# Kernel optimization log

Hardware: AMD Instinct MI355X
Metric: run time of the kernel (lower is better)

The kernel has to match this reference:

```python
import jax, jax.numpy as jnp
import numpy as np

B, N, D, H, F = 16, 512, 768, 8, 96  # D == H*F, dims preserved across layers
NEG_INF = -1e20


def setup_inputs() -> dict:
    key = jax.random.key(0)
    ks = jax.random.split(key, 16)
    embeddings = jax.random.normal(ks[0], (B, N, D), dtype=jnp.float32)
    # 0/1 float adjacency with self-loops so no row is fully masked
    adj = (jax.random.uniform(ks[1], (B, N, N)) < 0.3).astype(jnp.float32)
    adj = jnp.maximum(adj, jnp.eye(N, dtype=jnp.float32)[None])
    convo_len = jnp.full((B,), N, dtype=jnp.int32)

    def layer_params(k0, k1, k2, k3, k4, in_dim, out_dim):
        sW = (2.0 / (in_dim + out_dim)) ** 0.5  # ~xavier
        sa = (2.0 / (out_dim + 1)) ** 0.5
        sH = (2.0 / (in_dim + in_dim)) ** 0.5
        return dict(
            W=jax.random.normal(k0, (H, in_dim, out_dim)) * sW,
            b=jnp.zeros((out_dim,), jnp.float32),
            a_src=jax.random.normal(k1, (H, out_dim, 1)) * sa,
            a_dst=jax.random.normal(k2, (H, out_dim, 1)) * sa,
            Hw=jax.random.normal(k3, (in_dim, in_dim)) * sH,
            Hb=jnp.zeros((in_dim,), jnp.float32),
        )

    p0 = layer_params(ks[2], ks[3], ks[4], ks[5], ks[6], D, F)
    p1 = layer_params(ks[7], ks[8], ks[9], ks[10], ks[11], D, F)
    return {
        "embeddings": embeddings, "adj": adj, "convo_len": convo_len,
        "W0": p0["W"], "b0": p0["b"], "a_src0": p0["a_src"], "a_dst0": p0["a_dst"], "Hw0": p0["Hw"], "Hb0": p0["Hb"],
        "W1": p1["W"], "b1": p1["b"], "a_src1": p1["a_src"], "a_dst1": p1["a_dst"], "Hw1": p1["Hw"], "Hb1": p1["Hb"],
    }


def gat_layer(x, adj, W, b, a_src, a_dst, Hw, Hb):
    b_, n_, _ = x.shape
    h_, _, f_ = W.shape
    h = jnp.einsum('bni,hio->bhno', x, W)            # [B,H,N,F]
    t = jnp.tanh(h)
    s = jnp.einsum('bhno,ho->bhn', t, a_src[..., 0])  # attn_src
    d = jnp.einsum('bhno,ho->bhn', t, a_dst[..., 0])  # attn_dst
    attn = jax.nn.leaky_relu(s[:, :, :, None] + d[:, :, None, :], 0.2)  # [B,H,N,N]
    attn = jnp.where(adj[:, None, :, :] > 0, attn, NEG_INF)
    attn = jax.nn.softmax(attn, axis=-1)
    out = jnp.einsum('bhij,bhjo->bhio', attn, h) + b  # [B,H,N,F]
    # faithful to torch: transpose(0,1).contiguous().view(batch, N, -1)
    out = jnp.transpose(out, (1, 0, 2, 3)).reshape(b_, n_, h_ * f_)
    out = jax.nn.elu(out)
    gate = jax.nn.sigmoid(x @ Hw.T + Hb)
    return gate * out + (1.0 - gate) * x


def reference(embeddings, adj, convo_len,
              W0, b0, a_src0, a_dst0, Hw0, Hb0,
              W1, b1, a_src1, a_dst1, Hw1, Hb1):
    x = gat_layer(embeddings, adj, W0, b0, a_src0, a_dst0, Hw0, Hb0)
    x = gat_layer(x, adj, W1, b1, a_src1, a_dst1, Hw1, Hb1)
    return x
```

## Files before the change

kernel.cpp:

```cpp
#include <hip/hip_runtime.h>
#include <cstdint>
#include <cstddef>

typedef __attribute__((ext_vector_type(4))) float f32x4;
typedef __attribute__((ext_vector_type(8))) __bf16 bf16x8;
typedef __attribute__((ext_vector_type(8))) unsigned short u16x8;
typedef __attribute__((ext_vector_type(4))) unsigned short u16x4;

__device__ __forceinline__ unsigned short f2bf(float f){
  unsigned int u = __float_as_uint(f);
  u += 0x7fffu + ((u >> 16) & 1u);
  return (unsigned short)(u >> 16);
}
__device__ __forceinline__ float bf2f(unsigned short u){
  return __uint_as_float(((unsigned int)u) << 16);
}
__device__ __forceinline__ float fast_tanh(float x){
  const float e = __expf(2.f * x);
  return 1.f - 2.f / (e + 1.f);
}

__device__ __forceinline__ void gload_lds16(const void* g, void* l){
  __builtin_amdgcn_global_load_lds((const __attribute__((address_space(1))) void*)g,
                                   (__attribute__((address_space(3))) void*)l, 16, 0, 0);
}

__device__ __forceinline__ f32x4 mfma16(bf16x8 a, bf16x8 b, f32x4 c){
  return __builtin_amdgcn_mfma_f32_16x16x32_bf16(a, b, c, 0, 0, 0);
}

__global__ __launch_bounds__(256) void prep_kernel(const float* __restrict__ in,
                                                   unsigned short* __restrict__ out,
                                                   const float* __restrict__ adj,
                                                   unsigned int* __restrict__ mask){
  const int bid = blockIdx.x;
  if (bid < 6144){
    int i = bid * 256 + threadIdx.x;
    f32x4 v = ((const f32x4*)in)[i];
    union { unsigned short u[4]; unsigned long long ll; } o;
    #pragma unroll
    for (int e = 0; e < 4; ++e) o.u[e] = f2bf(v[e]);
    ((unsigned long long*)out)[i] = o.ll;
  } else {
    int idx = (bid - 6144) * 256 + threadIdx.x;
    const float* a = adj + (size_t)idx * 32;
    unsigned int m = 0;
    #pragma unroll
    for (int e = 0; e < 8; ++e){
      f32x4 v = *(const f32x4*)(a + e * 4);
      m |= (v[0] > 0.f ? 1u : 0u) << (e * 4);
      m |= (v[1] > 0.f ? 1u : 0u) << (e * 4 + 1);
      m |= (v[2] > 0.f ? 1u : 0u) << (e * 4 + 2);
      m |= (v[3] > 0.f ? 1u : 0u) << (e * 4 + 3);
    }
    mask[idx] = m;
  }
}

__global__ __launch_bounds__(192) void buildBt_kernel(const float* __restrict__ W0,
                                                      const float* __restrict__ Hw0,
                                                      unsigned short* __restrict__ Bt0,
                                                      const float* __restrict__ W1,
                                                      const float* __restrict__ Hw1,
                                                      unsigned short* __restrict__ Bt1){
  const int bid = blockIdx.x;
  const int layer = bid >= 1536;
  const int n = layer ? bid - 1536 : bid;
  const float* W  = layer ? W1  : W0;
  const float* Hw = layer ? Hw1 : Hw0;
  unsigned short* Bt = layer ? Bt1 : Bt0;
  int k4 = threadIdx.x;
  float v[4];
  if (n < 768){
    int head = n / 96, f = n % 96;
    const float* base = W + (size_t)head * 768 * 96 + f;
    #pragma unroll
    for (int e = 0; e < 4; ++e) v[e] = base[(size_t)(k4 * 4 + e) * 96];
  } else {
    f32x4 t = *(const f32x4*)(Hw + (size_t)(n - 768) * 768 + k4 * 4);
    #pragma unroll
    for (int e = 0; e < 4; ++e) v[e] = t[e];
  }
  union { unsigned short u[4]; unsigned long long ll; } o;
  #pragma unroll
  for (int e = 0; e < 4; ++e) o.u[e] = f2bf(v[e]);
  ((unsigned long long*)(Bt + (size_t)n * 768))[k4] = o.ll;
}

__global__ __launch_bounds__(256, 3)
void gemm_kernel(const unsigned short* __restrict__ A,
                 const unsigned short* __restrict__ Bt,
                 const float* __restrict__ Hb,
                 unsigned short* __restrict__ hb,
                 unsigned short* __restrict__ hT,
                 unsigned short* __restrict__ glogit){
  __shared__ __align__(16) char lds[49152];
  const int tid  = threadIdx.x;
  const int wid  = tid >> 6;
  const int lane = tid & 63;
  const int orig = blockIdx.x;
  const int wgid = (orig & 7) * 192 + (orig >> 3);
  const int mtile = wgid / 24, ntile = wgid % 24;
  const int m0 = mtile * 128, n0 = ntile * 64;
  const int wm = (wid >> 1) * 64, wn = (wid & 1) * 32;
  const int g = lane >> 4, r16 = lane & 15;

  auto stage = [&](int kt, char* base){
    #pragma unroll
    for (int c = 0; c < 4; ++c){
      const int ch = c * 256 + tid;
      const int row = ch >> 3, sp = ch & 7;
      const int cj = sp ^ (row & 7);
      gload_lds16(A + (size_t)(m0 + row) * 768 + kt * 64 + cj * 8, base + ch * 16);
    }
    #pragma unroll
    for (int c = 0; c < 2; ++c){
      const int ch = c * 256 + tid;
      const int row = ch >> 3, sp = ch & 7;
      const int cj = sp ^ (row & 7);
      gload_lds16(Bt + (size_t)(n0 + row) * 768 + kt * 64 + cj * 8, base + 16384 + ch * 16);
    }
  };

  f32x4 acc[4][2];
  #pragma unroll
  for (int i = 0; i < 4; ++i)
    #pragma unroll
    for (int j = 0; j < 2; ++j) acc[i][j] = (f32x4){0.f, 0.f, 0.f, 0.f};

  stage(0, lds);
  __syncthreads();

  for (int kt = 0; kt < 12; ++kt){
    const int cur = kt & 1;
    if (kt < 11) stage(kt + 1, lds + (cur ^ 1) * 24576);
    const char* base = lds + cur * 24576;
    bf16x8 af[4][2], bfr[2][2];
    #pragma unroll
    for (int t = 0; t < 4; ++t){
      const int rowA = wm + t * 16 + r16;
      #pragma unroll
      for (int kk = 0; kk < 2; ++kk){
        const int ckk = (kk << 2) | g;
        af[t][kk] = *(const bf16x8*)(base + rowA * 128 + ((ckk ^ (rowA & 7)) << 4));
      }
    }
    #pragma unroll
    for (int nt = 0; nt < 2; ++nt){
      const int rowB = wn + nt * 16 + r16;
      #pragma unroll
      for (int kk = 0; kk < 2; ++kk){
        const int ckk = (kk << 2) | g;
        bfr[nt][kk] = *(const bf16x8*)(base + 16384 + rowB * 128 + ((ckk ^ (rowB & 7)) << 4));
      }
    }
    #pragma unroll
    for (int mt = 0; mt < 4; ++mt)
      #pragma unroll
      for (int nt = 0; nt < 2; ++nt){
        acc[mt][nt] = mfma16(af[mt][0], bfr[nt][0], acc[mt][nt]);
        acc[mt][nt] = mfma16(af[mt][1], bfr[nt][1], acc[mt][nt]);
      }
    __syncthreads();
  }

  if (n0 < 768){
    #pragma unroll
    for (int mt = 0; mt < 4; ++mt){
      #pragma unroll
      for (int nt = 0; nt < 2; ++nt){
        const int n = n0 + wn + nt * 16 + r16;
        const int head = n / 96, f = n % 96;
        #pragma unroll
        for (int r = 0; r < 4; ++r){
          const int m = m0 + wm + mt * 16 + g * 4 + r;
          const unsigned short v = f2bf(acc[mt][nt][r]);
          hb[(size_t)m * 768 + n] = v;
          const int b = m >> 9, node = m & 511;
          hT[(((size_t)(b * 8 + head)) * 96 + f) * 512 + node] = v;
        }
      }
    }
  } else {
    #pragma unroll
    for (int mt = 0; mt < 4; ++mt){
      #pragma unroll
      for (int nt = 0; nt < 2; ++nt){
        const int n = n0 + wn + nt * 16 + r16;
        const float hbv = Hb[n - 768];
        #pragma unroll
        for (int r = 0; r < 4; ++r){
          const int m = m0 + wm + mt * 16 + g * 4 + r;
          glogit[(size_t)m * 768 + (n - 768)] = f2bf(acc[mt][nt][r] + hbv);
        }
      }
    }
  }
}

__global__ __launch_bounds__(256)
void sd_kernel(const unsigned short* __restrict__ h, const float* __restrict__ asrc,
               const float* __restrict__ adst, float* __restrict__ s, float* __restrict__ d){
  const int idx  = blockIdx.x * 4 + (threadIdx.x >> 6);
  const int lane = threadIdx.x & 63;
  const int m = idx >> 3, head = idx & 7;
  const unsigned short* hr = h + (size_t)m * 768 + head * 96;
  const float* as_ = asrc + head * 96;
  const float* ad_ = adst + head * 96;
  float t1 = fast_tanh(bf2f(hr[lane]));
  float ss = t1 * as_[lane];
  float dd = t1 * ad_[lane];
  if (lane < 32){
    float t2 = fast_tanh(bf2f(hr[64 + lane]));
    ss += t2 * as_[64 + lane];
    dd += t2 * ad_[64 + lane];
  }
  #pragma unroll
  for (int o = 32; o > 0; o >>= 1){ ss += __shfl_xor(ss, o); dd += __shfl_xor(dd, o); }
  if (lane == 0){
    const int b = m >> 9, node = m & 511;
    const int o = ((b * 8 + head) << 9) + node;
    s[o] = ss; d[o] = dd;
  }
}

__global__ __launch_bounds__(256)
void attn_kernel(const float* __restrict__ s, const float* __restrict__ d,
                 const unsigned int* __restrict__ mask,
                 const unsigned short* __restrict__ hT,
                 const float* __restrict__ bias,
                 const unsigned short* __restrict__ glogit,
                 const float* __restrict__ xin,
                 float* __restrict__ outf,
                 unsigned short* __restrict__ outb,
                 int write_b){
  const int idx = blockIdx.x;
  const int bh = idx & 127, ib = idx >> 7;
  const int b  = bh >> 3;
  const int tid = threadIdx.x, wid = tid >> 6, lane = tid & 63;
  const int g = lane >> 4, r16 = lane & 15;
  const int rowbase = ib * 64 + wid * 16;

  __shared__ float d_lds[512];
  __shared__ float bias_lds[96];
  __shared__ __align__(16) char vbuf[2][12288];
  float* att_s = (float*)vbuf;

  const float* dv = d + bh * 512;
  if (tid < 128) ((f32x4*)d_lds)[tid] = ((const f32x4*)dv)[tid];
  if (tid >= 128 && tid < 152) ((f32x4*)bias_lds)[tid - 128] = ((const f32x4*)bias)[tid - 128];

  const unsigned short* hTb = hT + (size_t)bh * 96 * 512;

  auto stage = [&](int p, int bufi){
    #pragma unroll
    for (int ss2 = 0; ss2 < 3; ++ss2){
      const int ch = ss2 * 256 + tid;
      const int row = ch >> 3, slotpos = ch & 7;
      const int cj = slotpos ^ (row & 7);
      gload_lds16(hTb + (size_t)row * 512 + p * 64 + cj * 8, vbuf[bufi] + ch * 16);
    }
  };

  const int i_mine = rowbase + r16;
  const float s_i = s[bh * 512 + i_mine];

  unsigned int mw[16];
  {
    const uint4* mrow = (const uint4*)(mask + ((size_t)b * 512 + i_mine) * 16);
    uint4 a0 = mrow[0], a1 = mrow[1], a2 = mrow[2], a3 = mrow[3];
    mw[0]=a0.x; mw[1]=a0.y; mw[2]=a0.z; mw[3]=a0.w;
    mw[4]=a1.x; mw[5]=a1.y; mw[6]=a1.z; mw[7]=a1.w;
    mw[8]=a2.x; mw[9]=a2.y; mw[10]=a2.z; mw[11]=a2.w;
    mw[12]=a3.x; mw[13]=a3.y; mw[14]=a3.z; mw[15]=a3.w;
  }

  stage(0, 0);
  __syncthreads();

  float Mx = d_lds[lane];
  #pragma unroll
  for (int t = 1; t < 8; ++t) Mx = fmaxf(Mx, d_lds[t * 64 + lane]);
  #pragma unroll
  for (int o = 32; o > 0; o >>= 1) Mx = fmaxf(Mx, __shfl_xor(Mx, o));
  const float scm = s_i + Mx;
  const float m_i = fmaxf(scm, 0.2f * scm);

  f32x4 acc2[6];
  #pragma unroll
  for (int ft = 0; ft < 6; ++ft) acc2[ft] = (f32x4){0.f, 0.f, 0.f, 0.f};
  float L = 0.f;

  for (int p = 0; p < 8; ++p){
    if (p < 7) stage(p + 1, (p + 1) & 1);
    const char* vb = vbuf[p & 1];
    #pragma unroll
    for (int half = 0; half < 2; ++half){
      const int jt = p * 2 + half;
      const unsigned int w = mw[jt];
      const int j8 = jt * 32 + g * 8;
      f32x4 dA = *(const f32x4*)(d_lds + j8);
      f32x4 dB = *(const f32x4*)(d_lds + j8 + 4);
      u16x8 pa;
      #pragma unroll
      for (int e = 0; e < 4; ++e){
        float sc = s_i + dA[e]; sc = fmaxf(sc, 0.2f * sc);
        float p1 = ((w >> (g * 8 + e)) & 1u) ? __expf(sc - m_i) : 0.f;
        L += p1; pa[e] = f2bf(p1);
        float sc2 = s_i + dB[e]; sc2 = fmaxf(sc2, 0.2f * sc2);
        float p2 = ((w >> (g * 8 + 4 + e)) & 1u) ? __expf(sc2 - m_i) : 0.f;
        L += p2; pa[4 + e] = f2bf(p2);
      }
      const bf16x8 af = __builtin_bit_cast(bf16x8, pa);
      const int slot = ((half * 4 + g) ^ (r16 & 7)) * 16;
      #pragma unroll
      for (int ft = 0; ft < 6; ++ft){
        bf16x8 vf = *(const bf16x8*)(vb + (ft * 16 + r16) * 128 + slot);
        acc2[ft] = mfma16(af, vf, acc2[ft]);
      }
    }
    __syncthreads();
  }

  L += __shfl_xor(L, 16);
  L += __shfl_xor(L, 32);
  const float linv = 1.f / L;
  float lr[4];
  #pragma unroll
  for (int r = 0; r < 4; ++r) lr[r] = __shfl(linv, g * 4 + r);

  #pragma unroll
  for (int ft = 0; ft < 6; ++ft){
    const int f = ft * 16 + r16;
    const float bv = bias_lds[f];
    #pragma unroll
    for (int r = 0; r < 4; ++r){
      const int node = rowbase + g * 4 + r;
      att_s[((node >> 3) & 7) * 768 + (node & 7) * 96 + f] = acc2[ft][r] * lr[r] + bv;
    }
  }
  __syncthreads();

  const int hh = bh & 7;
  const int bb2 = (hh << 1) | (b >> 3);
  const int mbase = bb2 * 512 + ((b & 7) << 6) + ib * 8;
  const size_t gb4 = (size_t)mbase * 192;
  #pragma unroll
  for (int sgi = 0; sgi < 6; ++sgi){
    const int ei = sgi * 256 + tid;
    f32x4 a4 = ((const f32x4*)att_s)[ei];
    u16x4 gl = ((const u16x4*)glogit)[gb4 + ei];
    f32x4 xv = ((const f32x4*)xin)[gb4 + ei];
    f32x4 o;
    #pragma unroll
    for (int e = 0; e < 4; ++e){
      const float gate = 1.f / (1.f + __expf(-bf2f(gl[e])));
      const float a = a4[e];
      const float eluv = a > 0.f ? a : (__expf(a) - 1.f);
      o[e] = gate * eluv + (1.f - gate) * xv[e];
    }
    ((f32x4*)outf)[gb4 + ei] = o;
    if (write_b){
      union { unsigned short u[4]; unsigned long long ll; } ob;
      #pragma unroll
      for (int e = 0; e < 4; ++e) ob.u[e] = f2bf(o[e]);
      ((unsigned long long*)outb)[gb4 + ei] = ob.ll;
    }
  }
}

extern "C" void kernel_launch(void* const* d_in, const int* in_sizes, int n_in,
                              void* d_out, int out_size, void* d_ws, size_t ws_size,
                              hipStream_t stream){
  const float* emb   = (const float*)d_in[0];
  const float* adj   = (const float*)d_in[1];
  const float* W0    = (const float*)d_in[3];
  const float* b0    = (const float*)d_in[4];
  const float* asrc0 = (const float*)d_in[5];
  const float* adst0 = (const float*)d_in[6];
  const float* Hw0   = (const float*)d_in[7];
  const float* Hb0   = (const float*)d_in[8];
  const float* W1    = (const float*)d_in[9];
  const float* b1    = (const float*)d_in[10];
  const float* asrc1 = (const float*)d_in[11];
  const float* adst1 = (const float*)d_in[12];
  const float* Hw1   = (const float*)d_in[13];
  const float* Hb1   = (const float*)d_in[14];

  char* ws = (char*)d_ws;
  size_t off = 0;
  auto alloc = [&](size_t bytes){ void* p = ws + off; off += (bytes + 255) & ~(size_t)255; return p; };
  unsigned short* x0b  = (unsigned short*)alloc(8192ull * 768 * 2);
  unsigned short* Bt0  = (unsigned short*)alloc(1536ull * 768 * 2);
  unsigned short* Bt1  = (unsigned short*)alloc(1536ull * 768 * 2);
  unsigned short* hb   = (unsigned short*)alloc(8192ull * 768 * 2);
  unsigned short* hT   = (unsigned short*)alloc(8192ull * 768 * 2);
  unsigned short* glogit = (unsigned short*)alloc(8192ull * 768 * 2);
  float* sbuf          = (float*)alloc(65536ull * 4);
  float* dbuf          = (float*)alloc(65536ull * 4);
  float* x1            = (float*)alloc(8192ull * 768 * 4);
  unsigned int* mask   = (unsigned int*)alloc(16ull * 512 * 16 * 4);
  (void)ws_size; (void)in_sizes; (void)n_in; (void)out_size;

  prep_kernel<<<6656, 256, 0, stream>>>(emb, x0b, adj, mask);
  buildBt_kernel<<<3072, 192, 0, stream>>>(W0, Hw0, Bt0, W1, Hw1, Bt1);

  gemm_kernel<<<1536, 256, 0, stream>>>(x0b, Bt0, Hb0, hb, hT, glogit);
  sd_kernel<<<16384, 256, 0, stream>>>(hb, asrc0, adst0, sbuf, dbuf);
  attn_kernel<<<1024, 256, 0, stream>>>(sbuf, dbuf, mask, hT, b0, glogit, emb, x1, x0b, 1);

  gemm_kernel<<<1536, 256, 0, stream>>>(x0b, Bt1, Hb1, hb, hT, glogit);
  sd_kernel<<<16384, 256, 0, stream>>>(hb, asrc1, adst1, sbuf, dbuf);
  attn_kernel<<<1024, 256, 0, stream>>>(sbuf, dbuf, mask, hT, b1, glogit, x1, (float*)d_out, x0b, 0);
}
```

Baseline: 288.4 us.

## Stage GEMM epilogue through LDS, drop hb buffer, rework sd kernel, merge prep

The GEMM epilogue now writes its tile into swizzled LDS and then issues 16-byte coalesced stores for both hT and glogit, replacing scattered 2-byte stores. The row-major hb copy is removed, and sd_kernel reads the transposed hT directly, with one block per (batch, head) and its attention vectors held in LDS. buildBt is merged into prep_kernel to save a launch, and s_setprio is raised around the MFMA loop in attention. The risks are extra LDS traffic and barriers in the epilogue, and that sd now runs only 128 blocks, which may underfill the GPU.

```diff
diff --git a/kernel.cpp b/kernel.cpp
--- a/kernel.cpp
+++ b/kernel.cpp
@@ -32,7 +32,13 @@
 __global__ __launch_bounds__(256) void prep_kernel(const float* __restrict__ in,
                                                    unsigned short* __restrict__ out,
                                                    const float* __restrict__ adj,
-                                                   unsigned int* __restrict__ mask){
+                                                   unsigned int* __restrict__ mask,
+                                                   const float* __restrict__ W0,
+                                                   const float* __restrict__ Hw0,
+                                                   unsigned short* __restrict__ Bt0,
+                                                   const float* __restrict__ W1,
+                                                   const float* __restrict__ Hw1,
+                                                   unsigned short* __restrict__ Bt1){
   const int bid = blockIdx.x;
   if (bid < 6144){
     int i = bid * 256 + threadIdx.x;
@@ -41,7 +47,7 @@
     #pragma unroll
     for (int e = 0; e < 4; ++e) o.u[e] = f2bf(v[e]);
     ((unsigned long long*)out)[i] = o.ll;
-  } else {
+  } else if (bid < 6656){
     int idx = (bid - 6144) * 256 + threadIdx.x;
     const float* a = adj + (size_t)idx * 32;
     unsigned int m = 0;
@@ -54,44 +60,38 @@
       m |= (v[3] > 0.f ? 1u : 0u) << (e * 4 + 3);
     }
     mask[idx] = m;
-  }
-}
-
-__global__ __launch_bounds__(192) void buildBt_kernel(const float* __restrict__ W0,
-                                                      const float* __restrict__ Hw0,
-                                                      unsigned short* __restrict__ Bt0,
-                                                      const float* __restrict__ W1,
-                                                      const float* __restrict__ Hw1,
-                                                      unsigned short* __restrict__ Bt1){
-  const int bid = blockIdx.x;
-  const int layer = bid >= 1536;
-  const int n = layer ? bid - 1536 : bid;
-  const float* W  = layer ? W1  : W0;
-  const float* Hw = layer ? Hw1 : Hw0;
-  unsigned short* Bt = layer ? Bt1 : Bt0;
-  int k4 = threadIdx.x;
-  float v[4];
-  if (n < 768){
-    int head = n / 96, f = n % 96;
-    const float* base = W + (size_t)head * 768 * 96 + f;
-    #pragma unroll
-    for (int e = 0; e < 4; ++e) v[e] = base[(size_t)(k4 * 4 + e) * 96];
   } else {
-    f32x4 t = *(const f32x4*)(Hw + (size_t)(n - 768) * 768 + k4 * 4);
-    #pragma unroll
-    for (int e = 0; e < 4; ++e) v[e] = t[e];
-  }
-  union { unsigned short u[4]; unsigned long long ll; } o;
-  #pragma unroll
-  for (int e = 0; e < 4; ++e) o.u[e] = f2bf(v[e]);
-  ((unsigned long long*)(Bt + (size_t)n * 768))[k4] = o.ll;
+    const int rel = bid - 6656;
+    const int layer = rel >= 1536;
+    const int n = layer ? rel - 1536 : rel;
+    const float* W  = layer ? W1  : W0;
+    const float* Hw = layer ? Hw1 : Hw0;
+    unsigned short* Bt = layer ? Bt1 : Bt0;
+    const int k4 = threadIdx.x;
+    if (k4 < 192){
+      float v[4];
+      if (n < 768){
+        int head = n / 96, f = n % 96;
+        const float* base = W + (size_t)head * 768 * 96 + f;
+        #pragma unroll
+        for (int e = 0; e < 4; ++e) v[e] = base[(size_t)(k4 * 4 + e) * 96];
+      } else {
+        f32x4 t = *(const f32x4*)(Hw + (size_t)(n - 768) * 768 + k4 * 4);
+        #pragma unroll
+        for (int e = 0; e < 4; ++e) v[e] = t[e];
+      }
+      union { unsigned short u[4]; unsigned long long ll; } o;
+      #pragma unroll
+      for (int e = 0; e < 4; ++e) o.u[e] = f2bf(v[e]);
+      ((unsigned long long*)(Bt + (size_t)n * 768))[k4] = o.ll;
+    }
+  }
 }
 
 __global__ __launch_bounds__(256, 3)
 void gemm_kernel(const unsigned short* __restrict__ A,
                  const unsigned short* __restrict__ Bt,
                  const float* __restrict__ Hb,
-                 unsigned short* __restrict__ hb,
                  unsigned short* __restrict__ hT,
                  unsigned short* __restrict__ glogit){
   __shared__ __align__(16) char lds[49152];
@@ -169,59 +169,82 @@
     for (int mt = 0; mt < 4; ++mt){
       #pragma unroll
       for (int nt = 0; nt < 2; ++nt){
-        const int n = n0 + wn + nt * 16 + r16;
-        const int head = n / 96, f = n % 96;
+        const int n_local = wn + nt * 16 + r16;
+        const int m_base  = wm + mt * 16 + g * 4;
+        union { unsigned short u[4]; unsigned long long ll; } pk;
+        #pragma unroll
+        for (int r = 0; r < 4; ++r) pk.u[r] = f2bf(acc[mt][nt][r]);
+        const int byte = m_base * 2;
+        const int chunk = byte >> 4, o = byte & 15;
+        const int pbyte = n_local * 256 + ((chunk ^ (n_local & 15)) << 4) + o;
+        *(unsigned long long*)(lds + pbyte) = pk.ll;
+      }
+    }
+    __syncthreads();
+    const int b_ = m0 >> 9, nodebase = m0 & 511;
+    #pragma unroll
+    for (int it = 0; it < 4; ++it){
+      const int ci = it * 256 + tid;
+      const int row = ci >> 4, l = ci & 15;
+      const int pbyte = row * 256 + (((l ^ (row & 15))) << 4);
+      f32x4 v = *(const f32x4*)(lds + pbyte);
+      const int n = n0 + row, head = n / 96, f = n % 96;
+      *(f32x4*)(hT + (((size_t)(b_ * 8 + head)) * 96 + f) * 512 + nodebase + l * 8) = v;
+    }
+  } else {
+    #pragma unroll
+    for (int mt = 0; mt < 4; ++mt){
+      #pragma unroll
+      for (int nt = 0; nt < 2; ++nt){
+        const int n_local = wn + nt * 16 + r16;
+        const float hbv = Hb[n0 - 768 + n_local];
+        const int c = n_local >> 3;
         #pragma unroll
         for (int r = 0; r < 4; ++r){
-          const int m = m0 + wm + mt * 16 + g * 4 + r;
-          const unsigned short v = f2bf(acc[mt][nt][r]);
-          hb[(size_t)m * 768 + n] = v;
-          const int b = m >> 9, node = m & 511;
-          hT[(((size_t)(b * 8 + head)) * 96 + f) * 512 + node] = v;
+          const int m_local = wm + mt * 16 + g * 4 + r;
+          const int pbyte = m_local * 128 + ((c ^ (m_local & 7)) << 4) + (n_local & 7) * 2;
+          *(unsigned short*)(lds + pbyte) = f2bf(acc[mt][nt][r] + hbv);
         }
       }
     }
-  } else {
-    #pragma unroll
-    for (int mt = 0; mt < 4; ++mt){
-      #pragma unroll
-      for (int nt = 0; nt < 2; ++nt){
-        const int n = n0 + wn + nt * 16 + r16;
-        const float hbv = Hb[n - 768];
-        #pragma unroll
-        for (int r = 0; r < 4; ++r){
-          const int m = m0 + wm + mt * 16 + g * 4 + r;
-          glogit[(size_t)m * 768 + (n - 768)] = f2bf(acc[mt][nt][r] + hbv);
-        }
-      }
+    __syncthreads();
+    const int colbase = n0 - 768;
+    #pragma unroll
+    for (int it = 0; it < 4; ++it){
+      const int ci = it * 256 + tid;
+      const int row = ci >> 3, l = ci & 7;
+      const int pbyte = row * 128 + ((l ^ (row & 7)) << 4);
+      f32x4 v = *(const f32x4*)(lds + pbyte);
+      *(f32x4*)(glogit + (size_t)(m0 + row) * 768 + colbase + l * 8) = v;
     }
   }
 }
 
 __global__ __launch_bounds__(256)
-void sd_kernel(const unsigned short* __restrict__ h, const float* __restrict__ asrc,
+void sd_kernel(const unsigned short* __restrict__ hT, const float* __restrict__ asrc,
                const float* __restrict__ adst, float* __restrict__ s, float* __restrict__ d){
-  const int idx  = blockIdx.x * 4 + (threadIdx.x >> 6);
-  const int lane = threadIdx.x & 63;
-  const int m = idx >> 3, head = idx & 7;
-  const unsigned short* hr = h + (size_t)m * 768 + head * 96;
-  const float* as_ = asrc + head * 96;
-  const float* ad_ = adst + head * 96;
-  float t1 = fast_tanh(bf2f(hr[lane]));
-  float ss = t1 * as_[lane];
-  float dd = t1 * ad_[lane];
-  if (lane < 32){
-    float t2 = fast_tanh(bf2f(hr[64 + lane]));
-    ss += t2 * as_[64 + lane];
-    dd += t2 * ad_[64 + lane];
-  }
-  #pragma unroll
-  for (int o = 32; o > 0; o >>= 1){ ss += __shfl_xor(ss, o); dd += __shfl_xor(dd, o); }
-  if (lane == 0){
-    const int b = m >> 9, node = m & 511;
-    const int o = ((b * 8 + head) << 9) + node;
-    s[o] = ss; d[o] = dd;
-  }
+  const int bh = blockIdx.x;
+  const int tid = threadIdx.x;
+  const int head = bh & 7;
+  __shared__ float as_lds[96], ad_lds[96];
+  if (tid < 96) as_lds[tid] = asrc[head * 96 + tid];
+  else if (tid >= 128 && tid < 224) ad_lds[tid - 128] = adst[head * 96 + tid - 128];
+  __syncthreads();
+
+  const unsigned short* hTb = hT + (size_t)bh * 96 * 512 + tid * 2;
+  float s0 = 0.f, s1 = 0.f, d0 = 0.f, d1 = 0.f;
+  #pragma unroll 8
+  for (int f = 0; f < 96; ++f){
+    const unsigned int u = *(const unsigned int*)(hTb + (size_t)f * 512);
+    const float t0 = fast_tanh(bf2f((unsigned short)(u & 0xffffu)));
+    const float t1 = fast_tanh(bf2f((unsigned short)(u >> 16)));
+    const float a = as_lds[f], dd = ad_lds[f];
+    s0 += t0 * a;  s1 += t1 * a;
+    d0 += t0 * dd; d1 += t1 * dd;
+  }
+  const int o = (bh << 9) + tid * 2;
+  *(float2*)(s + o) = make_float2(s0, s1);
+  *(float2*)(d + o) = make_float2(d0, d1);
 }
 
 __global__ __launch_bounds__(256)
@@ -313,11 +336,13 @@
       }
       const bf16x8 af = __builtin_bit_cast(bf16x8, pa);
       const int slot = ((half * 4 + g) ^ (r16 & 7)) * 16;
+      __builtin_amdgcn_s_setprio(1);
       #pragma unroll
       for (int ft = 0; ft < 6; ++ft){
         bf16x8 vf = *(const bf16x8*)(vb + (ft * 16 + r16) * 128 + slot);
         acc2[ft] = mfma16(af, vf, acc2[ft]);
       }
+      __builtin_amdgcn_s_setprio(0);
     }
     __syncthreads();
   }
@@ -393,7 +418,6 @@
   unsigned short* x0b  = (unsigned short*)alloc(8192ull * 768 * 2);
   unsigned short* Bt0  = (unsigned short*)alloc(1536ull * 768 * 2);
   unsigned short* Bt1  = (unsigned short*)alloc(1536ull * 768 * 2);
-  unsigned short* hb   = (unsigned short*)alloc(8192ull * 768 * 2);
   unsigned short* hT   = (unsigned short*)alloc(8192ull * 768 * 2);
   unsigned short* glogit = (unsigned short*)alloc(8192ull * 768 * 2);
   float* sbuf          = (float*)alloc(65536ull * 4);
@@ -402,14 +426,13 @@
   unsigned int* mask   = (unsigned int*)alloc(16ull * 512 * 16 * 4);
   (void)ws_size; (void)in_sizes; (void)n_in; (void)out_size;
 
-  prep_kernel<<<6656, 256, 0, stream>>>(emb, x0b, adj, mask);
-  buildBt_kernel<<<3072, 192, 0, stream>>>(W0, Hw0, Bt0, W1, Hw1, Bt1);
-
-  gemm_kernel<<<1536, 256, 0, stream>>>(x0b, Bt0, Hb0, hb, hT, glogit);
-  sd_kernel<<<16384, 256, 0, stream>>>(hb, asrc0, adst0, sbuf, dbuf);
+  prep_kernel<<<9728, 256, 0, stream>>>(emb, x0b, adj, mask, W0, Hw0, Bt0, W1, Hw1, Bt1);
+
+  gemm_kernel<<<1536, 256, 0, stream>>>(x0b, Bt0, Hb0, hT, glogit);
+  sd_kernel<<<128, 256, 0, stream>>>(hT, asrc0, adst0, sbuf, dbuf);
   attn_kernel<<<1024, 256, 0, stream>>>(sbuf, dbuf, mask, hT, b0, glogit, emb, x1, x0b, 1);
 
-  gemm_kernel<<<1536, 256, 0, stream>>>(x0b, Bt1, Hb1, hb, hT, glogit);
-  sd_kernel<<<16384, 256, 0, stream>>>(hb, asrc1, adst1, sbuf, dbuf);
+  gemm_kernel<<<1536, 256, 0, stream>>>(x0b, Bt1, Hb1, hT, glogit);
+  sd_kernel<<<128, 256, 0, stream>>>(hT, asrc1, adst1, sbuf, dbuf);
   attn_kernel<<<1024, 256, 0, stream>>>(sbuf, dbuf, mask, hT, b1, glogit, x1, (float*)d_out, x0b, 0);
 }
```

Result: faster. 248.2 us (-13.9%).
